# Kernel tuning notes

Measured on AMD Instinct MI355X. Metric: run time of the kernel, lower is better.

Reference implementation:

```python
import jax, jax.numpy as jnp
import numpy as np

B, T, O = 32, 2048, 18            # batch, triples per graph, hardcoded object count
DIN1, H, DOUT = 1500, 512, 512    # net1 input dim is hardcoded 1500 in the source

def _kaiming(key, fan_in, fan_out):
    return jax.random.normal(key, (fan_in, fan_out), jnp.float32) * np.sqrt(2.0 / fan_in)

def setup_inputs() -> dict:
    key = jax.random.key(0)
    ks = jax.random.split(key, 8)
    trip = jax.random.normal(ks[0], (B, T, DIN1), jnp.float32)
    index = jax.random.randint(ks[1], (B, T, 2), 0, O)
    rel_lens = jax.random.randint(ks[2], (B,), 0, T)
    # net1: 1500 -> H -> 2H+Dout (ReLU after every layer incl. last)
    w1a = _kaiming(ks[3], DIN1, H); b1a = jnp.zeros((H,), jnp.float32)
    w1b = _kaiming(ks[4], H, 2 * H + DOUT); b1b = jnp.zeros((2 * H + DOUT,), jnp.float32)
    # net2: H -> H -> Dout (ReLU after every layer incl. last)
    w2a = _kaiming(ks[5], H, H); b2a = jnp.zeros((H,), jnp.float32)
    w2b = _kaiming(ks[6], H, DOUT); b2b = jnp.zeros((DOUT,), jnp.float32)
    return dict(trip=trip, index=index, rel_lens=rel_lens,
                w1a=w1a, b1a=b1a, w1b=w1b, b1b=b1b,
                w2a=w2a, b2a=b2a, w2b=w2b, b2b=b2b)

def reference(trip, index, rel_lens, w1a, b1a, w1b, b1b, w2a, b2a, w2b, b2b):
    # net1 MLP over all triples: [B,T,1500] -> [B,T,2H+Dout]
    h = jax.nn.relu(trip @ w1a + b1a)
    new_t = jax.nn.relu(h @ w1b + b1b)
    s_vecs = new_t[..., :H]              # [B,T,H] subject
    p_vecs = new_t[..., H:H + DOUT]      # [B,T,Dout] predicate (returned as-is)
    o_vecs = new_t[..., H + DOUT:]       # [B,T,H] object
    # mask out triples beyond rel_lens[i]
    mask = (jnp.arange(T)[None, :] < rel_lens[:, None]).astype(new_t.dtype)  # [B,T]
    oh_s = jax.nn.one_hot(index[..., 0], O, dtype=new_t.dtype) * mask[..., None]  # [B,T,O]
    oh_o = jax.nn.one_hot(index[..., 1], O, dtype=new_t.dtype) * mask[..., None]
    # per-batch scatter_add pooling into the O=18 object slots
    contrib = (jnp.einsum('bto,bth->boh', oh_s, s_vecs)
               + jnp.einsum('bto,bth->boh', oh_o, o_vecs))  # [B,O,H]
    # original code never resets pooled_obj_vecs inside the batch loop ->
    # accumulation is CUMULATIVE over batch items
    pooled = jnp.cumsum(contrib, axis=0)  # [B,O,H]
    # net2 MLP on each cumulative pool
    h2 = jax.nn.relu(pooled @ w2a + b2a)
    new_obj = jax.nn.relu(h2 @ w2b + b2b)  # [B,O,Dout]
    return new_obj, p_vecs
```

## Files before the change

kernel.cpp:

```cpp
#include <hip/hip_runtime.h>
#include <hip/hip_bf16.h>

#define NBATCH 32
#define NTIME  2048
#define NOBJ   18
#define KIN    1500
#define NH     512
#define NTOT   1536
#define NM     65536

typedef __attribute__((ext_vector_type(4))) float f32x4;
typedef __attribute__((ext_vector_type(8))) short s16x8;
typedef __attribute__((ext_vector_type(4))) short s16x4;

static __device__ __forceinline__ short f2bf(float f) {
  union { float f; unsigned u; } v; v.f = f;
  unsigned r = v.u + 0x7fffu + ((v.u >> 16) & 1u);
  return (short)(r >> 16);
}

static __device__ __forceinline__ void gload_lds16(const short* g, short* l) {
  __builtin_amdgcn_global_load_lds(
      (const __attribute__((address_space(1))) unsigned int*)(g),
      (__attribute__((address_space(3))) unsigned int*)(l), 16, 0, 0);
}

#define FENCE() asm volatile("" ::: "memory")
#define BAR()   do { FENCE(); __builtin_amdgcn_s_barrier(); FENCE(); } while (0)
#define LGKM0() asm volatile("s_waitcnt lgkmcnt(0)" ::: "memory")

__global__ void k_prep(const float* __restrict__ src, short* __restrict__ dst,
                       int K, int Nsrc, int nkt, int total) {
  int i = blockIdx.x * 256 + threadIdx.x;
  if (i >= total) return;
  int chunk = i >> 14, off = i & 16383;
  int row = off >> 6, kcp = off & 63;
  int kc = kcp ^ ((row & 7) << 3);
  int cb = chunk / nkt, kt = chunk - cb * nkt;
  int n = cb * 256 + row, k = kt * 64 + kc;
  dst[i] = (k < K) ? f2bf(src[(size_t)k * Nsrc + n]) : (short)0;
}

__global__ void k_zero(float* __restrict__ p, int n) {
  int i = blockIdx.x * 256 + threadIdx.x;
  if (i < n) p[i] = 0.f;
}

__launch_bounds__(512, 2)
__global__ void k_gemm1(const float* __restrict__ A, const short* __restrict__ Bc,
                        const float* __restrict__ bias, short* __restrict__ Hc) {
  __shared__ short lA[2][256 * 64];
  __shared__ short lB[2][256 * 64];
  const int g = blockIdx.x;
  const int lid = (g & 7) * 64 + (g >> 3);
  const int rb = lid >> 1, cb = lid & 1;
  const int m0 = rb * 256, n0 = cb * 256;
  const int tid = threadIdx.x;
  const int lane = tid & 63, w = tid >> 6;
  const int wr = w >> 2, wc = w & 3;
  const int rlane = lane & 15, ksel = (lane >> 4) * 8;
  const int swz = (rlane & 7) << 3;
  const int kx0 = ksel ^ swz, kx1 = (32 | ksel) ^ swz;
  const int arow = tid >> 4;
  const int akq  = (tid & 15) * 4;
  const short* bchunk = Bc + (size_t)(cb * 24) * 16384;

  f32x4 acc[8][4] = {};
  float4 av0[4], av1[4];
  s16x8 af[4][2];
  s16x8 bf0[2][2], bf1[2][2];

  auto issueA_h = [&](int kt, int h, float4 (&av)[4]) {
    const int kbase = kt * 64;
    const bool fullq = (kt < 23) | (akq <= 24);
#pragma unroll
    for (int i = 0; i < 4; ++i) {
      const float* p = A + (size_t)(m0 + arow + (h * 4 + i) * 32) * KIN + kbase + akq;
      av[i] = fullq ? *(const float4*)p : make_float4(0.f, 0.f, 0.f, 0.f);
    }
  };
  auto writeA_h = [&](int nb, int h, float4 (&av)[4]) {
#pragma unroll
    for (int i = 0; i < 4; ++i) {
      int r = arow + (h * 4 + i) * 32;
      s16x4 h4;
      h4[0] = f2bf(av[i].x); h4[1] = f2bf(av[i].y);
      h4[2] = f2bf(av[i].z); h4[3] = f2bf(av[i].w);
      *(s16x4*)&lA[nb][r * 64 + (akq ^ ((r & 7) << 3))] = h4;
    }
  };
  auto issueB_full = [&](int nb, int kt) {
    const short* src = bchunk + (size_t)kt * 16384 + tid * 8;
#pragma unroll
    for (int j = 0; j < 4; ++j)
      gload_lds16(src + j * 4096, &lB[nb][tid * 8 + j * 4096]);
  };
  auto readA = [&](int cu, int rh) {
#pragma unroll
    for (int mm = 0; mm < 4; ++mm) {
      int ro = (rh * 128 + wr * 64 + mm * 16 + rlane) * 64;
      af[mm][0] = *(const s16x8*)&lA[cu][ro + kx0];
      af[mm][1] = *(const s16x8*)&lA[cu][ro + kx1];
    }
  };
  auto readB = [&](int cu, int ch, s16x8 (&dst)[2][2]) {
#pragma unroll
    for (int qn = 0; qn < 2; ++qn) {
      int ro = (ch * 128 + wc * 32 + qn * 16 + rlane) * 64;
      dst[qn][0] = *(const s16x8*)&lB[cu][ro + kx0];
      dst[qn][1] = *(const s16x8*)&lB[cu][ro + kx1];
    }
  };
  auto mfma_quad = [&](int rh, int ch, s16x8 (&bfr)[2][2]) {
    __builtin_amdgcn_s_setprio(1);
#pragma unroll
    for (int j = 0; j < 2; ++j)
#pragma unroll
      for (int mm = 0; mm < 4; ++mm)
#pragma unroll
        for (int qn = 0; qn < 2; ++qn)
          acc[rh * 4 + mm][ch * 2 + qn] = __builtin_amdgcn_mfma_f32_16x16x32_bf16(
              af[mm][j], bfr[qn][j], acc[rh * 4 + mm][ch * 2 + qn], 0, 0, 0);
    __builtin_amdgcn_s_setprio(0);
  };

  issueA_h(0, 0, av0);
  issueA_h(0, 1, av1);
  issueB_full(0, 0);
  writeA_h(0, 0, av0);
  writeA_h(0, 1, av1);
  issueA_h(1, 0, av0);
  issueA_h(1, 1, av1);
  asm volatile("s_waitcnt vmcnt(8)" ::: "memory");
  LGKM0();
  BAR();

#pragma unroll 1
  for (int kt = 0; kt < 24; ++kt) {
    const int cu = kt & 1, nb = cu ^ 1;
    readA(cu, 0); readB(cu, 0, bf0);
    if (kt < 23) issueB_full(nb, kt + 1);
    mfma_quad(0, 0, bf0);
    readB(cu, 1, bf1);
    if (kt < 23) writeA_h(nb, 0, av0);
    mfma_quad(0, 1, bf1);
    readA(cu, 1);
    if (kt < 22) issueA_h(kt + 2, 0, av0);
    mfma_quad(1, 1, bf1);
    if (kt < 23) writeA_h(nb, 1, av1);
    if (kt < 22) issueA_h(kt + 2, 1, av1);
    mfma_quad(1, 0, bf0);
    if (kt < 23) {
      if (kt < 22) { asm volatile("s_waitcnt vmcnt(8)" ::: "memory"); }
      else         { asm volatile("s_waitcnt vmcnt(0)" ::: "memory"); }
      LGKM0();
      BAR();
    }
  }

#pragma unroll
  for (int n = 0; n < 4; ++n) {
    int c = n0 + (n >> 1) * 128 + wc * 32 + (n & 1) * 16 + rlane;
    float bv = bias[c];
#pragma unroll
    for (int m = 0; m < 8; ++m) {
      int rbase = m0 + (m >> 2) * 128 + wr * 64 + (m & 3) * 16 + ((lane >> 4) << 2);
#pragma unroll
      for (int q = 0; q < 4; ++q) {
        int r = rbase + q;
        float v = acc[m][n][q] + bv;
        v = v > 0.f ? v : 0.f;
        Hc[(size_t)(((r >> 8) * 8 + (c >> 6)) * 16384) + (r & 255) * 64 +
           ((c & 63) ^ ((r & 7) << 3))] = f2bf(v);
      }
    }
  }
}

__launch_bounds__(512, 2)
__global__ void k_gemm2(const short* __restrict__ Ac, const short* __restrict__ Bc,
                        const float* __restrict__ bias, const int* __restrict__ index,
                        const int* __restrict__ rel_lens,
                        float* __restrict__ contrib, float* __restrict__ out) {
  __shared__ short lA[2][256 * 64];
  __shared__ short lB[2][256 * 64];
  const int g = blockIdx.x;
  const int lid = (g & 7) * 192 + (g >> 3);
  const int rb = lid / 6, cb = lid - rb * 6;
  const int m0 = rb * 256;
  const int tid = threadIdx.x;
  const int lane = tid & 63, w = tid >> 6;
  const int wr = w >> 2, wc = w & 3;
  const int rlane = lane & 15, ksel = (lane >> 4) * 8;
  const int swz = (rlane & 7) << 3;
  const int kx0 = ksel ^ swz, kx1 = (32 | ksel) ^ swz;
  const short* achunk = Ac + (size_t)(rb * 8) * 16384;
  const short* bchunk = Bc + (size_t)(cb * 8) * 16384;

  f32x4 acc[8][4] = {};
  s16x8 af[4][2], bf0[2][2], bf1[2][2];

  auto issueA_full = [&](int nb, int kt) {
    const short* src = achunk + (size_t)kt * 16384 + tid * 8;
#pragma unroll
    for (int j = 0; j < 4; ++j)
      gload_lds16(src + j * 4096, &lA[nb][tid * 8 + j * 4096]);
  };
  auto issueB_full = [&](int nb, int kt) {
    const short* src = bchunk + (size_t)kt * 16384 + tid * 8;
#pragma unroll
    for (int j = 0; j < 4; ++j)
      gload_lds16(src + j * 4096, &lB[nb][tid * 8 + j * 4096]);
  };
  auto readA = [&](int cu, int rh) {
#pragma unroll
    for (int mm = 0; mm < 4; ++mm) {
      int ro = (rh * 128 + wr * 64 + mm * 16 + rlane) * 64;
      af[mm][0] = *(const s16x8*)&lA[cu][ro + kx0];
      af[mm][1] = *(const s16x8*)&lA[cu][ro + kx1];
    }
  };
  auto readB = [&](int cu, int ch, s16x8 (&dst)[2][2]) {
#pragma unroll
    for (int qn = 0; qn < 2; ++qn) {
      int ro = (ch * 128 + wc * 32 + qn * 16 + rlane) * 64;
      dst[qn][0] = *(const s16x8*)&lB[cu][ro + kx0];
      dst[qn][1] = *(const s16x8*)&lB[cu][ro + kx1];
    }
  };
  auto mfma_quad = [&](int rh, int ch, s16x8 (&bfr)[2][2]) {
    __builtin_amdgcn_s_setprio(1);
#pragma unroll
    for (int j = 0; j < 2; ++j)
#pragma unroll
      for (int mm = 0; mm < 4; ++mm)
#pragma unroll
        for (int qn = 0; qn < 2; ++qn)
          acc[rh * 4 + mm][ch * 2 + qn] = __builtin_amdgcn_mfma_f32_16x16x32_bf16(
              af[mm][j], bfr[qn][j], acc[rh * 4 + mm][ch * 2 + qn], 0, 0, 0);
    __builtin_amdgcn_s_setprio(0);
  };

  issueA_full(0, 0);
  issueB_full(0, 0);
  asm volatile("s_waitcnt vmcnt(0)" ::: "memory");
  BAR();

#pragma unroll 1
  for (int kt = 0; kt < 8; ++kt) {
    const int cu = kt & 1, nb = cu ^ 1;
    readA(cu, 0); readB(cu, 0, bf0);
    if (kt < 7) { issueA_full(nb, kt + 1); issueB_full(nb, kt + 1); }
    mfma_quad(0, 0, bf0);
    readB(cu, 1, bf1);
    mfma_quad(0, 1, bf1);
    readA(cu, 1);
    mfma_quad(1, 1, bf1);
    mfma_quad(1, 0, bf0);
    if (kt < 7) {
      asm volatile("s_waitcnt vmcnt(0)" ::: "memory");
      BAR();
    }
  }

  const int region = cb >> 1;
  float bv[4]; int cg[4];
#pragma unroll
  for (int n = 0; n < 4; ++n) {
    cg[n] = cb * 256 + (n >> 1) * 128 + wc * 32 + (n & 1) * 16 + rlane;
    bv[n] = bias[cg[n]];
  }

  if (region == 1) {
    float* po = out + (size_t)NBATCH * NOBJ * NH;
#pragma unroll
    for (int m = 0; m < 8; ++m) {
      int rbase = m0 + (m >> 2) * 128 + wr * 64 + (m & 3) * 16 + ((lane >> 4) << 2);
#pragma unroll
      for (int q = 0; q < 4; ++q) {
#pragma unroll
        for (int n = 0; n < 4; ++n) {
          float v = acc[m][n][q] + bv[n];
          v = v > 0.f ? v : 0.f;
          po[(size_t)(rbase + q) * NH + (cg[n] & 511)] = v;
        }
      }
    }
  } else {
    const int sel = region >> 1;
    const int b = m0 >> 11;
    const int rel = rel_lens[b];
#pragma unroll
    for (int m = 0; m < 8; ++m) {
      int rbase = m0 + (m >> 2) * 128 + wr * 64 + (m & 3) * 16 + ((lane >> 4) << 2);
#pragma unroll
      for (int q = 0; q < 4; ++q) {
        int r = rbase + q;
        if ((r & 2047) < rel) {
          int idx = index[2 * r + sel];
          float* dst = contrib + ((b * NOBJ + idx) << 9);
#pragma unroll
          for (int n = 0; n < 4; ++n) {
            float v = acc[m][n][q] + bv[n];
            v = v > 0.f ? v : 0.f;
            atomicAdd(dst + (cg[n] & 511), v);
          }
        }
      }
    }
  }
}

__global__ void k_cumsum(const float* __restrict__ contrib, float* __restrict__ pooled) {
  int i = blockIdx.x * 256 + threadIdx.x;
  if (i >= NOBJ * NH) return;
  float a = 0.f;
#pragma unroll
  for (int b = 0; b < NBATCH; ++b) {
    a += contrib[b * (NOBJ * NH) + i];
    pooled[b * (NOBJ * NH) + i] = a;
  }
}

__global__ void k_mlp2(const float* __restrict__ pooled,
                       const float* __restrict__ w2a, const float* __restrict__ b2a,
                       const float* __restrict__ w2b, const float* __restrict__ b2b,
                       float* __restrict__ out) {
  __shared__ float pr[NH];
  __shared__ float hr[NH];
  int row = blockIdx.x;
  int tid = threadIdx.x;
  pr[tid]       = pooled[(size_t)row * NH + tid];
  pr[tid + 256] = pooled[(size_t)row * NH + tid + 256];
  __syncthreads();
  float s0 = 0.f, s1 = 0.f;
  for (int k = 0; k < NH; ++k) {
    float p = pr[k];
    s0 += p * w2a[k * NH + tid];
    s1 += p * w2a[k * NH + tid + 256];
  }
  s0 += b2a[tid]; s1 += b2a[tid + 256];
  hr[tid]       = s0 > 0.f ? s0 : 0.f;
  hr[tid + 256] = s1 > 0.f ? s1 : 0.f;
  __syncthreads();
  s0 = 0.f; s1 = 0.f;
  for (int k = 0; k < NH; ++k) {
    float h = hr[k];
    s0 += h * w2b[k * NH + tid];
    s1 += h * w2b[k * NH + tid + 256];
  }
  s0 += b2b[tid]; s1 += b2b[tid + 256];
  out[(size_t)row * NH + tid]       = s0 > 0.f ? s0 : 0.f;
  out[(size_t)row * NH + tid + 256] = s1 > 0.f ? s1 : 0.f;
}

extern "C" void kernel_launch(void* const* d_in, const int* in_sizes, int n_in,
                              void* d_out, int out_size, void* d_ws, size_t ws_size,
                              hipStream_t stream) {
  const float* trip     = (const float*)d_in[0];
  const int*   index    = (const int*)d_in[1];
  const int*   rel_lens = (const int*)d_in[2];
  const float* w1a      = (const float*)d_in[3];
  const float* b1a      = (const float*)d_in[4];
  const float* w1b      = (const float*)d_in[5];
  const float* b1b      = (const float*)d_in[6];
  const float* w2a      = (const float*)d_in[7];
  const float* b2a      = (const float*)d_in[8];
  const float* w2b      = (const float*)d_in[9];
  const float* b2b      = (const float*)d_in[10];
  float* out = (float*)d_out;

  char* ws = (char*)d_ws;
  short* wt1a    = (short*)(ws);
  short* wt1b    = (short*)(ws + 1572864);
  short* hbuf    = (short*)(ws + 3145728);
  float* contrib = (float*)(ws + 70254592);
  float* pooled  = contrib + NBATCH * NOBJ * NH;

  k_prep<<<3072, 256, 0, stream>>>(w1a, wt1a, KIN, NH, 24, NH * 1536);
  k_prep<<<3072, 256, 0, stream>>>(w1b, wt1b, NH, NTOT, 8, NTOT * NH);
  k_zero<<<1152, 256, 0, stream>>>(contrib, NBATCH * NOBJ * NH);
  k_gemm1<<<512, 512, 0, stream>>>(trip, wt1a, b1a, hbuf);
  k_gemm2<<<1536, 512, 0, stream>>>(hbuf, wt1b, b1b, index, rel_lens, contrib, out);
  k_cumsum<<<36, 256, 0, stream>>>(contrib, pooled);
  k_mlp2<<<576, 256, 0, stream>>>(pooled, w2a, b2a, w2b, b2b, out);
}
```

Measured before the change: 501.3 us.

## Pre-convert activations to swizzled bf16 tiles and async-load them in gemm1

Adds a separate kernel that converts the fp32 triple input into bf16 tiles with the same swizzled layout used for LDS, stored in workspace. gemm1 then streams both A and B tiles directly into LDS with global_load_lds instead of loading fp32 into registers, converting, and writing LDS. This simplifies the gemm1 pipeline and frees registers. In exchange it adds an extra full pass writing and rereading a converted copy of the large input, and the prefetch distance for A shrinks to one tile.

```diff
diff --git a/kernel.cpp b/kernel.cpp
--- a/kernel.cpp
+++ b/kernel.cpp
@@ -27,7 +27,6 @@
 
 #define FENCE() asm volatile("" ::: "memory")
 #define BAR()   do { FENCE(); __builtin_amdgcn_s_barrier(); FENCE(); } while (0)
-#define LGKM0() asm volatile("s_waitcnt lgkmcnt(0)" ::: "memory")
 
 __global__ void k_prep(const float* __restrict__ src, short* __restrict__ dst,
                        int K, int Nsrc, int nkt, int total) {
@@ -41,13 +40,35 @@
   dst[i] = (k < K) ? f2bf(src[(size_t)k * Nsrc + n]) : (short)0;
 }
 
+__global__ void k_prepA(const float* __restrict__ src, short* __restrict__ dst) {
+  int i = blockIdx.x * 256 + threadIdx.x;
+  int chunk = i >> 11;
+  int off = i & 2047;
+  int row = off >> 3, g = off & 7;
+  int rb = chunk / 24, kt = chunk - rb * 24;
+  int gs = g ^ (row & 7);
+  int m = rb * 256 + row;
+  int k0 = kt * 64 + gs * 8;
+  const float* p = src + (size_t)m * KIN + k0;
+  s16x8 o;
+  if (k0 + 8 <= KIN) {
+    float4 a = *(const float4*)p, b = *(const float4*)(p + 4);
+    o[0] = f2bf(a.x); o[1] = f2bf(a.y); o[2] = f2bf(a.z); o[3] = f2bf(a.w);
+    o[4] = f2bf(b.x); o[5] = f2bf(b.y); o[6] = f2bf(b.z); o[7] = f2bf(b.w);
+  } else {
+#pragma unroll
+    for (int j = 0; j < 8; ++j) o[j] = (k0 + j < KIN) ? f2bf(p[j]) : (short)0;
+  }
+  *(s16x8*)&dst[(size_t)chunk * 16384 + off * 8] = o;
+}
+
 __global__ void k_zero(float* __restrict__ p, int n) {
   int i = blockIdx.x * 256 + threadIdx.x;
   if (i < n) p[i] = 0.f;
 }
 
 __launch_bounds__(512, 2)
-__global__ void k_gemm1(const float* __restrict__ A, const short* __restrict__ Bc,
+__global__ void k_gemm1(const short* __restrict__ Ac, const short* __restrict__ Bc,
                         const float* __restrict__ bias, short* __restrict__ Hc) {
   __shared__ short lA[2][256 * 64];
   __shared__ short lB[2][256 * 64];
@@ -61,33 +82,17 @@
   const int rlane = lane & 15, ksel = (lane >> 4) * 8;
   const int swz = (rlane & 7) << 3;
   const int kx0 = ksel ^ swz, kx1 = (32 | ksel) ^ swz;
-  const int arow = tid >> 4;
-  const int akq  = (tid & 15) * 4;
+  const short* achunk = Ac + (size_t)(rb * 24) * 16384;
   const short* bchunk = Bc + (size_t)(cb * 24) * 16384;
 
   f32x4 acc[8][4] = {};
-  float4 av0[4], av1[4];
-  s16x8 af[4][2];
-  s16x8 bf0[2][2], bf1[2][2];
-
-  auto issueA_h = [&](int kt, int h, float4 (&av)[4]) {
-    const int kbase = kt * 64;
-    const bool fullq = (kt < 23) | (akq <= 24);
-#pragma unroll
-    for (int i = 0; i < 4; ++i) {
-      const float* p = A + (size_t)(m0 + arow + (h * 4 + i) * 32) * KIN + kbase + akq;
-      av[i] = fullq ? *(const float4*)p : make_float4(0.f, 0.f, 0.f, 0.f);
-    }
-  };
-  auto writeA_h = [&](int nb, int h, float4 (&av)[4]) {
-#pragma unroll
-    for (int i = 0; i < 4; ++i) {
-      int r = arow + (h * 4 + i) * 32;
-      s16x4 h4;
-      h4[0] = f2bf(av[i].x); h4[1] = f2bf(av[i].y);
-      h4[2] = f2bf(av[i].z); h4[3] = f2bf(av[i].w);
-      *(s16x4*)&lA[nb][r * 64 + (akq ^ ((r & 7) << 3))] = h4;
-    }
+  s16x8 af[4][2], bf0[2][2], bf1[2][2];
+
+  auto issueA_full = [&](int nb, int kt) {
+    const short* src = achunk + (size_t)kt * 16384 + tid * 8;
+#pragma unroll
+    for (int j = 0; j < 4; ++j)
+      gload_lds16(src + j * 4096, &lA[nb][tid * 8 + j * 4096]);
   };
   auto issueB_full = [&](int nb, int kt) {
     const short* src = bchunk + (size_t)kt * 16384 + tid * 8;
@@ -124,36 +129,24 @@
     __builtin_amdgcn_s_setprio(0);
   };
 
-  issueA_h(0, 0, av0);
-  issueA_h(0, 1, av1);
+  issueA_full(0, 0);
   issueB_full(0, 0);
-  writeA_h(0, 0, av0);
-  writeA_h(0, 1, av1);
-  issueA_h(1, 0, av0);
-  issueA_h(1, 1, av1);
-  asm volatile("s_waitcnt vmcnt(8)" ::: "memory");
-  LGKM0();
+  asm volatile("s_waitcnt vmcnt(0)" ::: "memory");
   BAR();
 
 #pragma unroll 1
   for (int kt = 0; kt < 24; ++kt) {
     const int cu = kt & 1, nb = cu ^ 1;
     readA(cu, 0); readB(cu, 0, bf0);
-    if (kt < 23) issueB_full(nb, kt + 1);
+    if (kt < 23) { issueA_full(nb, kt + 1); issueB_full(nb, kt + 1); }
     mfma_quad(0, 0, bf0);
     readB(cu, 1, bf1);
-    if (kt < 23) writeA_h(nb, 0, av0);
     mfma_quad(0, 1, bf1);
     readA(cu, 1);
-    if (kt < 22) issueA_h(kt + 2, 0, av0);
     mfma_quad(1, 1, bf1);
-    if (kt < 23) writeA_h(nb, 1, av1);
-    if (kt < 22) issueA_h(kt + 2, 1, av1);
     mfma_quad(1, 0, bf0);
     if (kt < 23) {
-      if (kt < 22) { asm volatile("s_waitcnt vmcnt(8)" ::: "memory"); }
-      else         { asm volatile("s_waitcnt vmcnt(0)" ::: "memory"); }
-      LGKM0();
+      asm volatile("s_waitcnt vmcnt(0)" ::: "memory");
       BAR();
     }
   }
@@ -376,11 +369,13 @@
   short* hbuf    = (short*)(ws + 3145728);
   float* contrib = (float*)(ws + 70254592);
   float* pooled  = contrib + NBATCH * NOBJ * NH;
-
+  short* abuf    = (short*)(ws + 75497472);
+
+  k_zero<<<1152, 256, 0, stream>>>(contrib, NBATCH * NOBJ * NH);
   k_prep<<<3072, 256, 0, stream>>>(w1a, wt1a, KIN, NH, 24, NH * 1536);
   k_prep<<<3072, 256, 0, stream>>>(w1b, wt1b, NH, NTOT, 8, NTOT * NH);
-  k_zero<<<1152, 256, 0, stream>>>(contrib, NBATCH * NOBJ * NH);
-  k_gemm1<<<512, 512, 0, stream>>>(trip, wt1a, b1a, hbuf);
+  k_prepA<<<49152, 256, 0, stream>>>(trip, abuf);
+  k_gemm1<<<512, 512, 0, stream>>>(abuf, wt1a, b1a, hbuf);
   k_gemm2<<<1536, 512, 0, stream>>>(hbuf, wt1b, b1b, index, rel_lens, contrib, out);
   k_cumsum<<<36, 256, 0, stream>>>(contrib, pooled);
   k_mlp2<<<576, 256, 0, stream>>>(pooled, w2a, b2a, w2b, b2b, out);
```

After: 529.5 us. +5.6%, slower.
